# Optimization experiments

Measured on AMD Instinct MI355X. Metric: run time of the kernel, lower is better.

Reference implementation:

```python
import jax, jax.numpy as jnp
import numpy as np

B, N = 4, 1024                 # images, proposals per image
C_IN, POOL, HID = 256, 7, 1024
NUM_CLASSES = 21               # 20 fg + background (include_bg=False => +1)
FEAT_DIM = C_IN * POOL * POOL  # 12544
IMAGE_H = IMAGE_W = 800.0
STDS = np.array([0.1, 0.1, 0.2, 0.2], np.float32)
SCORE_THRESH = 0.1
NMS_THRESH = 0.5


def setup_inputs():
    key = jax.random.key(0)
    ks = jax.random.split(key, 11)
    props_feature = jax.random.normal(ks[0], (B * N, FEAT_DIM), jnp.float32)
    # well-formed xyxy proposals inside the image
    xy = jax.random.uniform(ks[1], (B, N, 2), minval=0.0, maxval=IMAGE_W - 64.0)
    wh = jax.random.uniform(ks[2], (B, N, 2), minval=8.0, maxval=256.0)
    proposals = jnp.concatenate([xy, jnp.minimum(xy + wh, IMAGE_W)], axis=-1)
    s = 0.02
    return {
        'props_feature': props_feature,
        'proposals': proposals,
        'fc6_w': jax.random.normal(ks[3], (FEAT_DIM, HID), jnp.float32) * s,
        'fc6_b': jnp.zeros((HID,), jnp.float32),
        'fc7_w': jax.random.normal(ks[4], (HID, HID), jnp.float32) * s,
        'fc7_b': jnp.zeros((HID,), jnp.float32),
        'cls_w': jax.random.normal(ks[5], (HID, NUM_CLASSES), jnp.float32) * s,
        'cls_b': jnp.zeros((NUM_CLASSES,), jnp.float32),
        'box_w': jax.random.normal(ks[6], (HID, NUM_CLASSES * 4), jnp.float32) * s,
        'box_b': jnp.zeros((NUM_CLASSES * 4,), jnp.float32),
    }


def _decode(deltas, props):
    # NormalizedProposalDecoder: deltas [...,4] (normalized), props xyxy [...,4]
    d = deltas * jnp.asarray(STDS)  # means are 0
    w = props[..., 2] - props[..., 0]
    h = props[..., 3] - props[..., 1]
    cx = props[..., 0] + 0.5 * w
    cy = props[..., 1] + 0.5 * h
    pcx = d[..., 0] * w + cx
    pcy = d[..., 1] * h + cy
    pw = jnp.exp(d[..., 2]) * w
    ph = jnp.exp(d[..., 3]) * h
    return jnp.stack([pcx - 0.5 * pw, pcy - 0.5 * ph,
                      pcx + 0.5 * pw, pcy + 0.5 * ph], axis=-1)


def _pairwise_iou(a, b):
    lt = jnp.maximum(a[:, None, :2], b[None, :, :2])
    rb = jnp.minimum(a[:, None, 2:], b[None, :, 2:])
    wh = jnp.maximum(rb - lt, 0.0)
    inter = wh[..., 0] * wh[..., 1]
    area_a = (a[:, 2] - a[:, 0]) * (a[:, 3] - a[:, 1])
    area_b = (b[:, 2] - b[:, 0]) * (b[:, 3] - b[:, 1])
    return inter / jnp.maximum(area_a[:, None] + area_b[None, :] - inter, 1e-9)


def _nms_keep(boxes, scores, labels, valid):
    # torchvision batched_nms: per-class via coordinate offset trick
    sc = jnp.where(valid, scores, -1.0)
    order = jnp.argsort(-sc)
    off = labels[order].astype(boxes.dtype)[:, None] * (IMAGE_W + 1.0)
    b = boxes[order] + off
    iou = _pairwise_iou(b, b)  # [N, N]
    idx = jnp.arange(N)

    def body(i, keep):
        sup = (iou[i] > NMS_THRESH) & keep[i] & (idx > i)
        return keep & ~sup

    keep_sorted = jax.lax.fori_loop(0, N, body, valid[order])
    return jnp.zeros(N, bool).at[order].set(keep_sorted)


def reference(props_feature, proposals, fc6_w, fc6_b, fc7_w, fc7_b,
              cls_w, cls_b, box_w, box_b):
    # TwoMLPHead
    x = jax.nn.relu(props_feature @ fc6_w + fc6_b)
    x = jax.nn.relu(x @ fc7_w + fc7_b)
    # FastRCNNPredictor
    scores = jax.nn.softmax(x @ cls_w + cls_b, axis=-1).reshape(B, N, NUM_CLASSES)
    deltas = (x @ box_w + box_b).reshape(B, N, NUM_CLASSES, 4)
    boxes = _decode(deltas, proposals[:, :, None, :])  # [B,N,C,4]
    # drop background column, keep per-box max-score class (scores == max mask)
    sc_fg = scores[..., 1:]
    bx_fg = boxes[:, :, 1:, :]
    best = jnp.argmax(sc_fg, axis=-1)                                  # [B,N]
    sc = jnp.take_along_axis(sc_fg, best[..., None], axis=-1)[..., 0]
    bx = jnp.take_along_axis(bx_fg, best[..., None, None], axis=-2)[..., 0, :]
    labels = best + 1
    # BBoxClipToImageSize
    hi = jnp.asarray([IMAGE_W, IMAGE_H, IMAGE_W, IMAGE_H], bx.dtype)
    bx = jnp.clip(bx, jnp.zeros(4, bx.dtype), hi)
    # BBoxSizeFilter(min=0) + score threshold
    valid = ((bx[..., 2] - bx[..., 0] > 0.0) & (bx[..., 3] - bx[..., 1] > 0.0)
             & (sc > SCORE_THRESH))
    keep = jax.vmap(_nms_keep)(bx, sc, labels, valid)                  # [B,N]
    res = jnp.concatenate([bx, (labels - 1).astype(bx.dtype)[..., None],
                           sc[..., None]], axis=-1)                    # [B,N,6]
    res = jnp.where(keep[..., None], res, 0.0)  # padded in place of ragged lists
    rpn_props = jnp.pad(proposals, ((0, 0), (0, 0), (0, 2)))
    rcnn_props = jnp.pad(bx, ((0, 0), (0, 0), (0, 2)))
    return res, keep, rpn_props, rcnn_props
```

## Files before the change

### kernel.cpp

```cpp
#include <hip/hip_runtime.h>
#include <hip/hip_bf16.h>

#define BATCH 4
#define NPROP 1024
#define HID 1024
#define NUM_CLASSES 21
#define FEAT_DIM 12544
#define NPB (BATCH * NPROP)
#define IMG 800.0f
#define SCORE_THRESH 0.1f
#define NMS_THRESH 0.5f
#define NCOL 112

typedef unsigned short u16;
typedef unsigned int u32;
typedef unsigned long long u64;
typedef short s16x8 __attribute__((ext_vector_type(8)));
typedef float f32x4 __attribute__((ext_vector_type(4)));

__device__ __forceinline__ void split2(float x0, float x1, u32& hp, u32& lp) {
    __hip_bfloat162 h2 = __float22bfloat162_rn(make_float2(x0, x1));
    u32 h = *(u32*)&h2;
    float f0 = __uint_as_float(h << 16);
    float f1 = __uint_as_float(h & 0xffff0000u);
    __hip_bfloat162 l2 = __float22bfloat162_rn(make_float2(x0 - f0, x1 - f1));
    hp = h;
    lp = *(u32*)&l2;
}

__device__ __forceinline__ size_t tile_off(int blk, int NTt, int t, int row, int g) {
    int r = row & 127;
    int c = r >> 4;
    int lanei = ((r & 15) << 2) | (g ^ ((r >> 1) & 3));
    return ((((size_t)blk * NTt + t) * 8 + c) << 9) + lanei * 8;
}

#define NB_WCAT 448
#define NB_T7C  256
#define NB_T6C  3136
#define NB_SPA  2048
#define NB_PREP (NB_WCAT + NB_T7C + NB_T6C + NB_SPA)

__device__ __forceinline__ void w_chunks(
    const float* __restrict__ W, u16* __restrict__ Th, u16* __restrict__ Tl,
    int NTt, int nb, int t, int tid, float (*lt)[129])
{
    const int n0 = nb * 128;
#pragma unroll
    for (int p = 0; p < 4; ++p) {
        int e = (p * 256 + tid) * 4;
        int k = e >> 7;
        int n = e & 127;
        float4 v = *(const float4*)(W + (size_t)(t * 32 + k) * 1024 + n0 + n);
        lt[k][n] = v.x; lt[k][n + 1] = v.y; lt[k][n + 2] = v.z; lt[k][n + 3] = v.w;
    }
    __syncthreads();
    const int lane = tid & 63, w = tid >> 6;
#pragma unroll
    for (int i = 0; i < 2; ++i) {
        const int c = w * 2 + i;
        const int rl = c * 16 + (lane >> 2);
        const int q = (lane & 3) ^ ((rl >> 1) & 3);
        u32 hp[4], lp[4];
#pragma unroll
        for (int e2 = 0; e2 < 4; ++e2)
            split2(lt[q * 8 + 2 * e2][rl], lt[q * 8 + 2 * e2 + 1][rl], hp[e2], lp[e2]);
        const size_t dsto = ((((size_t)nb * NTt + t) * 8 + c) << 9) + lane * 8;
        *(uint4*)&Th[dsto] = make_uint4(hp[0], hp[1], hp[2], hp[3]);
        *(uint4*)&Tl[dsto] = make_uint4(lp[0], lp[1], lp[2], lp[3]);
    }
    __syncthreads();
}

__global__ __launch_bounds__(256) void prep_kernel(
    const float* __restrict__ fc6_w, const float* __restrict__ fc7_w,
    const float* __restrict__ cls_w, const float* __restrict__ box_w,
    const float* __restrict__ A,
    u16* __restrict__ W6h, u16* __restrict__ W6l,
    u16* __restrict__ W7h, u16* __restrict__ W7l,
    float* __restrict__ Wcat, u16* __restrict__ A6h, u16* __restrict__ A6l)
{
    __shared__ float lt[32][129];
    const int b = blockIdx.x;
    const int tid = threadIdx.x;

    if (b < NB_WCAT) {
        int i = b * 256 + tid;
        if (i < HID * NCOL) {
            int k = i / NCOL, c = i % NCOL;
            float v = 0.0f;
            if (c < 21) v = cls_w[k * 21 + c];
            else if (c < 105) v = box_w[k * 84 + (c - 21)];
            Wcat[i] = v;
        }
    } else if (b < NB_WCAT + NB_T7C) {
        int idx = b - NB_WCAT;
        w_chunks(fc7_w, W7h, W7l, 32, idx / 32, idx % 32, tid, lt);
    } else if (b < NB_WCAT + NB_T7C + NB_T6C) {
        int idx = b - NB_WCAT - NB_T7C;
        w_chunks(fc6_w, W6h, W6l, 392, idx / 392, idx % 392, tid, lt);
    } else {
        const int sb = b - NB_WCAT - NB_T7C - NB_T6C;
        const int lane = tid & 63;
        const int w = tid >> 6;
        const int NCH = (NPB / 128) * (FEAT_DIM / 32) * 8;
        const int STRIDE = NB_SPA * 4;
        const int STRIDE4 = STRIDE * 4;

        auto srcaddr = [&](int ch) -> const float* {
            const int c = ch & 7;
            const int tmp = ch >> 3;
            const int t = tmp % (FEAT_DIM / 32);
            const int blk = tmp / (FEAT_DIM / 32);
            const int r = blk * 128 + c * 16 + (lane >> 2);
            const int col = t * 32 + (((lane & 3) ^ ((r >> 1) & 3)) << 3);
            return A + (size_t)r * FEAT_DIM + col;
        };
        auto proc = [&](int ch, const float4& xx, const float4& yy) {
            u32 hp0, hp1, hp2, hp3, lp0, lp1, lp2, lp3;
            split2(xx.x, xx.y, hp0, lp0);
            split2(xx.z, xx.w, hp1, lp1);
            split2(yy.x, yy.y, hp2, lp2);
            split2(yy.z, yy.w, hp3, lp3);
            const size_t dsto = ((size_t)ch << 9) + lane * 8;
            *(uint4*)&A6h[dsto] = make_uint4(hp0, hp1, hp2, hp3);
            *(uint4*)&A6l[dsto] = make_uint4(lp0, lp1, lp2, lp3);
        };

        int c0 = sb * 4 + w;
        int c1 = c0 + STRIDE;
        int c2 = c1 + STRIDE;
        int c3 = c2 + STRIDE;
        float4 x0{}, y0{}, x1{}, y1{}, x2{}, y2{}, x3{}, y3{};
        { const float* s = srcaddr(c0); x0 = *(const float4*)s; y0 = *(const float4*)(s + 4); }
        { const float* s = srcaddr(c1); x1 = *(const float4*)s; y1 = *(const float4*)(s + 4); }
        { const float* s = srcaddr(c2); x2 = *(const float4*)s; y2 = *(const float4*)(s + 4); }
        { const float* s = srcaddr(c3); x3 = *(const float4*)s; y3 = *(const float4*)(s + 4); }

        while (c0 < NCH || c1 < NCH || c2 < NCH || c3 < NCH) {
            if (c0 < NCH) {
                proc(c0, x0, y0);
                c0 += STRIDE4;
                if (c0 < NCH) { const float* s = srcaddr(c0); x0 = *(const float4*)s; y0 = *(const float4*)(s + 4); }
            }
            if (c1 < NCH) {
                proc(c1, x1, y1);
                c1 += STRIDE4;
                if (c1 < NCH) { const float* s = srcaddr(c1); x1 = *(const float4*)s; y1 = *(const float4*)(s + 4); }
            }
            if (c2 < NCH) {
                proc(c2, x2, y2);
                c2 += STRIDE4;
                if (c2 < NCH) { const float* s = srcaddr(c2); x2 = *(const float4*)s; y2 = *(const float4*)(s + 4); }
            }
            if (c3 < NCH) {
                proc(c3, x3, y3);
                c3 += STRIDE4;
                if (c3 < NCH) { const float* s = srcaddr(c3); x3 = *(const float4*)s; y3 = *(const float4*)(s + 4); }
            }
        }
    }
}

__global__ __launch_bounds__(256) void transpose_split(
    const float* __restrict__ W, u16* __restrict__ WhT, u16* __restrict__ WlT,
    int K, int N)
{
    __shared__ float tile[32][33];
    const int tid = threadIdx.x;
    const int n0 = blockIdx.x * 32;
    const int k0 = blockIdx.y * 32;
    {
        int i = tid >> 3, j4 = (tid & 7) * 4;
        float4 v = *(const float4*)(W + (size_t)(k0 + i) * N + n0 + j4);
        tile[i][j4] = v.x; tile[i][j4 + 1] = v.y; tile[i][j4 + 2] = v.z; tile[i][j4 + 3] = v.w;
    }
    __syncthreads();
    {
        int i = tid >> 3, j4 = (tid & 7) * 4;
        u32 hp0, lp0, hp1, lp1;
        split2(tile[j4 + 0][i], tile[j4 + 1][i], hp0, lp0);
        split2(tile[j4 + 2][i], tile[j4 + 3][i], hp1, lp1);
        size_t o = (size_t)(n0 + i) * K + k0 + j4;
        *(uint2*)&WhT[o] = make_uint2(hp0, hp1);
        *(uint2*)&WlT[o] = make_uint2(lp0, lp1);
    }
}

__global__ void build_wcat(const float* __restrict__ cls_w, const float* __restrict__ box_w,
                           float* __restrict__ Wcat)
{
    int i = blockIdx.x * 256 + threadIdx.x;
    if (i >= HID * NCOL) return;
    int k = i / NCOL, c = i % NCOL;
    float v = 0.0f;
    if (c < 21) v = cls_w[k * 21 + c];
    else if (c < 105) v = box_w[k * 84 + (c - 21)];
    Wcat[i] = v;
}

__global__ __launch_bounds__(256) void gemm_2ph_tiled(
    const u16* __restrict__ Ah, const u16* __restrict__ Al,
    const u16* __restrict__ Wh, const u16* __restrict__ Wl,
    const float* __restrict__ bias, float* __restrict__ Cout,
    int M, int Nn, int NTt, int tN, int mb0, int ymask, int bzshift)
{
    __shared__ u16 sm[2 * 16384];

    const int tid = threadIdx.x;
    const int lane = tid & 63;
    const int wv = tid >> 6;
    const int wr = wv >> 1, wc = wv & 1;

    const int flat = blockIdx.x + (blockIdx.y << 3) + blockIdx.z * 8 * gridDim.y;
    const int xcd = flat & 7;
    const int j = flat >> 3;
    const int bxi = j & 7;
    const int yy = (j >> 3) & ymask;
    const int bz = j >> bzshift;
    const int mb = mb0 + xcd * (ymask + 1) + yy;
    const int nb = bxi;
    const int bm = mb * 128, bn = nb * 128;
    const int t0 = bz * tN;

    const size_t abase = (size_t)mb * NTt * 4096;
    const size_t wbase = (size_t)nb * NTt * 4096;

    const int fr = lane & 15, fq = lane >> 4;
    int ia[4], ib[4];
#pragma unroll
    for (int m = 0; m < 4; ++m) {
        int ra = wr * 64 + m * 16 + fr;
        ia[m] = ra * 32 + ((fq ^ ((ra >> 1) & 3)) << 3);
        int rb = wc * 64 + m * 16 + fr;
        ib[m] = rb * 32 + ((fq ^ ((rb >> 1) & 3)) << 3);
    }

    f32x4 acc[4][4];
#pragma unroll
    for (int m = 0; m < 4; ++m)
#pragma unroll
        for (int n = 0; n < 4; ++n)
            acc[m][n] = (f32x4){0.f, 0.f, 0.f, 0.f};

    auto stage = [&](u16* dst, int t) {
#pragma unroll
        for (int i = 0; i < 2; ++i) {
            const int c = wv * 2 + i;
            const size_t so = (((size_t)t * 8 + c) << 9) + lane * 8;
            __builtin_amdgcn_global_load_lds(
                (const __attribute__((address_space(1))) u32*)(Ah + abase + so),
                (__attribute__((address_space(3))) u32*)(dst + c * 512), 16, 0, 0);
            __builtin_amdgcn_global_load_lds(
                (const __attribute__((address_space(1))) u32*)(Al + abase + so),
                (__attribute__((address_space(3))) u32*)(dst + 4096 + c * 512), 16, 0, 0);
            __builtin_amdgcn_global_load_lds(
                (const __attribute__((address_space(1))) u32*)(Wh + wbase + so),
                (__attribute__((address_space(3))) u32*)(dst + 8192 + c * 512), 16, 0, 0);
            __builtin_amdgcn_global_load_lds(
                (const __attribute__((address_space(1))) u32*)(Wl + wbase + so),
                (__attribute__((address_space(3))) u32*)(dst + 12288 + c * 512), 16, 0, 0);
        }
    };

    auto compute = [&](const u16* src) {
        s16x8 fah[4], fal[4], fbh[4], fbl[4];
#pragma unroll
        for (int m = 0; m < 4; ++m) {
            fah[m] = *(const s16x8*)&src[ia[m]];
            fal[m] = *(const s16x8*)&src[4096 + ia[m]];
            fbh[m] = *(const s16x8*)&src[8192 + ib[m]];
            fbl[m] = *(const s16x8*)&src[12288 + ib[m]];
        }
        __builtin_amdgcn_s_setprio(1);
#pragma unroll
        for (int m = 0; m < 4; ++m)
#pragma unroll
            for (int n = 0; n < 4; ++n) {
                acc[m][n] = __builtin_amdgcn_mfma_f32_16x16x32_bf16(fah[m], fbh[n], acc[m][n], 0, 0, 0);
                acc[m][n] = __builtin_amdgcn_mfma_f32_16x16x32_bf16(fah[m], fbl[n], acc[m][n], 0, 0, 0);
                acc[m][n] = __builtin_amdgcn_mfma_f32_16x16x32_bf16(fal[m], fbh[n], acc[m][n], 0, 0, 0);
            }
        __builtin_amdgcn_s_setprio(0);
    };

    u16* bufc = sm;
    u16* bufn = sm + 16384;

    stage(bufc, t0);
    for (int t = 0; t < tN; ++t) {
        if (t + 1 < tN) {
            stage(bufn, t0 + t + 1);
            asm volatile("s_waitcnt vmcnt(8)" ::: "memory");
        } else {
            asm volatile("s_waitcnt vmcnt(0)" ::: "memory");
        }
        asm volatile("s_barrier" ::: "memory");
        compute(bufc);
        asm volatile("s_barrier" ::: "memory");
        u16* tmp = bufc; bufc = bufn; bufn = tmp;
    }

    if (bias != nullptr) {
#pragma unroll
        for (int n = 0; n < 4; ++n) {
            int col = bn + wc * 64 + n * 16 + fr;
            float bb = bias[col];
#pragma unroll
            for (int m = 0; m < 4; ++m) {
                int row0 = bm + wr * 64 + m * 16 + fq * 4;
#pragma unroll
                for (int jj = 0; jj < 4; ++jj)
                    Cout[(size_t)(row0 + jj) * Nn + col] = fmaxf(acc[m][n][jj] + bb, 0.0f);
            }
        }
    } else {
        float* Cp = Cout + (size_t)bz * M * Nn;
#pragma unroll
        for (int n = 0; n < 4; ++n) {
            int col = bn + wc * 64 + n * 16 + fr;
#pragma unroll
            for (int m = 0; m < 4; ++m) {
                int row0 = bm + wr * 64 + m * 16 + fq * 4;
#pragma unroll
                for (int jj = 0; jj < 4; ++jj)
                    Cp[(size_t)(row0 + jj) * Nn + col] = acc[m][n][jj];
            }
        }
    }
}

__global__ __launch_bounds__(256) void gemm_2ph(
    const float* __restrict__ A, const u16* __restrict__ WhT, const u16* __restrict__ WlT,
    const float* __restrict__ bias, float* __restrict__ Cout,
    int M, int Nn, int K, int KC)
{
    __shared__ u16 sm[2 * 16384];

    const int tid = threadIdx.x;
    const int lane = tid & 63;
    const int wv = tid >> 6;
    const int wr = wv >> 1, wc = wv & 1;

    const int flat = blockIdx.x + (blockIdx.y << 3) + (blockIdx.z << 8);
    const int xcd = flat & 7;
    const int j = flat >> 3;
    const int bxi = j & 7;
    const int yy = (j >> 3) & 3;
    const int bz = j >> 5;
    const int bm = (xcd * 4 + yy) * 128;
    const int bn = bxi * 128;
    const int k0 = bz * KC;
    const int NT = KC / 32;

    const int ar = tid >> 1;
    const int ah = tid & 1;
    const float* aPtr = A + (size_t)(bm + ar) * K + ah * 16;
    const int asw = (ar >> 1) & 3;
    const int ac0 = ((2 * ah) ^ asw) << 3;
    const int ac1 = ((2 * ah + 1) ^ asw) << 3;

    int wrow[2], wlc[2];
#pragma unroll
    for (int i = 0; i < 2; ++i) {
        int c = wv * 2 + i;
        wrow[i] = c * 16 + (lane >> 2);
        wlc[i] = ((lane & 3) ^ ((wrow[i] >> 1) & 3)) * 8;
    }

    const int fr = lane & 15, fq = lane >> 4;
    int ia[4], ib[4];
#pragma unroll
    for (int m = 0; m < 4; ++m) {
        int ra = wr * 64 + m * 16 + fr;
        ia[m] = ra * 32 + ((fq ^ ((ra >> 1) & 3)) << 3);
        int rb = wc * 64 + m * 16 + fr;
        ib[m] = rb * 32 + ((fq ^ ((rb >> 1) & 3)) << 3);
    }

    f32x4 acc[4][4];
#pragma unroll
    for (int m = 0; m < 4; ++m)
#pragma unroll
        for (int n = 0; n < 4; ++n)
            acc[m][n] = (f32x4){0.f, 0.f, 0.f, 0.f};

    auto stage_w = [&](u16* dst, int kk) {
#pragma unroll
        for (int i = 0; i < 2; ++i) {
            const int c = wv * 2 + i;
            const u16* gh = WhT + (size_t)(bn + wrow[i]) * K + kk + wlc[i];
            const u16* gl = WlT + (size_t)(bn + wrow[i]) * K + kk + wlc[i];
            __builtin_amdgcn_global_load_lds(
                (const __attribute__((address_space(1))) u32*)gh,
                (__attribute__((address_space(3))) u32*)(dst + 8192 + c * 512), 16, 0, 0);
            __builtin_amdgcn_global_load_lds(
                (const __attribute__((address_space(1))) u32*)gl,
                (__attribute__((address_space(3))) u32*)(dst + 12288 + c * 512), 16, 0, 0);
        }
    };

    auto split_a = [&](u16* dst, float4 v0, float4 v1, float4 v2, float4 v3) {
        u32 hp[8], lp[8];
        split2(v0.x, v0.y, hp[0], lp[0]);
        split2(v0.z, v0.w, hp[1], lp[1]);
        split2(v1.x, v1.y, hp[2], lp[2]);
        split2(v1.z, v1.w, hp[3], lp[3]);
        split2(v2.x, v2.y, hp[4], lp[4]);
        split2(v2.z, v2.w, hp[5], lp[5]);
        split2(v3.x, v3.y, hp[6], lp[6]);
        split2(v3.z, v3.w, hp[7], lp[7]);
        *(uint4*)&dst[ar * 32 + ac0] = make_uint4(hp[0], hp[1], hp[2], hp[3]);
        *(uint4*)&dst[ar * 32 + ac1] = make_uint4(hp[4], hp[5], hp[6], hp[7]);
        *(uint4*)&dst[4096 + ar * 32 + ac0] = make_uint4(lp[0], lp[1], lp[2], lp[3]);
        *(uint4*)&dst[4096 + ar * 32 + ac1] = make_uint4(lp[4], lp[5], lp[6], lp[7]);
    };

    auto compute = [&](const u16* src) {
        s16x8 fah[4], fal[4], fbh[4], fbl[4];
#pragma unroll
        for (int m = 0; m < 4; ++m) {
            fah[m] = *(const s16x8*)&src[ia[m]];
            fal[m] = *(const s16x8*)&src[4096 + ia[m]];
            fbh[m] = *(const s16x8*)&src[8192 + ib[m]];
            fbl[m] = *(const s16x8*)&src[12288 + ib[m]];
        }
        __builtin_amdgcn_s_setprio(1);
#pragma unroll
        for (int m = 0; m < 4; ++m)
#pragma unroll
            for (int n = 0; n < 4; ++n) {
                acc[m][n] = __builtin_amdgcn_mfma_f32_16x16x32_bf16(fah[m], fbh[n], acc[m][n], 0, 0, 0);
                acc[m][n] = __builtin_amdgcn_mfma_f32_16x16x32_bf16(fah[m], fbl[n], acc[m][n], 0, 0, 0);
                acc[m][n] = __builtin_amdgcn_mfma_f32_16x16x32_bf16(fal[m], fbh[n], acc[m][n], 0, 0, 0);
            }
        __builtin_amdgcn_s_setprio(0);
    };

    u16* bufc = sm;
    u16* bufn = sm + 16384;

    stage_w(bufc, k0);
    {
        float4 a0 = *(const float4*)(aPtr + k0 + 0);
        float4 a1 = *(const float4*)(aPtr + k0 + 4);
        float4 a2 = *(const float4*)(aPtr + k0 + 8);
        float4 a3 = *(const float4*)(aPtr + k0 + 12);
        split_a(bufc, a0, a1, a2, a3);
    }
    asm volatile("s_waitcnt vmcnt(0) lgkmcnt(0)\n\ts_barrier" ::: "memory");

    for (int t = 0; t < NT; ++t) {
        float4 a0{}, a1{}, a2{}, a3{};
        const bool hn = (t + 1 < NT);
        if (hn) {
            const int kk = k0 + (t + 1) * 32;
            stage_w(bufn, kk);
            a0 = *(const float4*)(aPtr + kk + 0);
            a1 = *(const float4*)(aPtr + kk + 4);
            a2 = *(const float4*)(aPtr + kk + 8);
            a3 = *(const float4*)(aPtr + kk + 12);
        }
        compute(bufc);
        if (hn) split_a(bufn, a0, a1, a2, a3);
        asm volatile("s_waitcnt vmcnt(0) lgkmcnt(0)\n\ts_barrier" ::: "memory");
        u16* tmp = bufc; bufc = bufn; bufn = tmp;
    }

    if (bias != nullptr) {
#pragma unroll
        for (int n = 0; n < 4; ++n) {
            int col = bn + wc * 64 + n * 16 + fr;
            float bb = bias[col];
#pragma unroll
            for (int m = 0; m < 4; ++m) {
                int row0 = bm + wr * 64 + m * 16 + fq * 4;
#pragma unroll
                for (int jj = 0; jj < 4; ++jj)
                    Cout[(size_t)(row0 + jj) * Nn + col] = fmaxf(acc[m][n][jj] + bb, 0.0f);
            }
        }
    } else {
        float* Cp = Cout + (size_t)bz * M * Nn;
#pragma unroll
        for (int n = 0; n < 4; ++n) {
            int col = bn + wc * 64 + n * 16 + fr;
#pragma unroll
            for (int m = 0; m < 4; ++m) {
                int row0 = bm + wr * 64 + m * 16 + fq * 4;
#pragma unroll
                for (int jj = 0; jj < 4; ++jj)
                    Cp[(size_t)(row0 + jj) * Nn + col] = acc[m][n][jj];
            }
        }
    }
}

__global__ __launch_bounds__(256) void reduce_bias_relu(
    const float* __restrict__ Cpart, const float* __restrict__ bias,
    float* __restrict__ X, int MN, int Nn)
{
    const int total = MN / 4;
    for (int i4 = blockIdx.x * 256 + threadIdx.x; i4 < total; i4 += gridDim.x * 256) {
        const size_t o = (size_t)i4 * 4;
        float4 a = *(const float4*)(Cpart + o);
        float4 b = *(const float4*)(Cpart + (size_t)MN + o);
        float4 c = *(const float4*)(Cpart + 2 * (size_t)MN + o);
        float4 d = *(const float4*)(Cpart + 3 * (size_t)MN + o);
        float4 bb = *(const float4*)(bias + (o & (size_t)(Nn - 1)));
        float4 r;
        r.x = fmaxf(a.x + b.x + c.x + d.x + bb.x, 0.0f);
        r.y = fmaxf(a.y + b.y + c.y + d.y + bb.y, 0.0f);
        r.z = fmaxf(a.z + b.z + c.z + d.z + bb.z, 0.0f);
        r.w = fmaxf(a.w + b.w + c.w + d.w + bb.w, 0.0f);
        *(float4*)(X + o) = r;
    }
}

__global__ __launch_bounds__(256) void reduce_split_tiled(
    const float* __restrict__ Cpart, const float* __restrict__ bias,
    u16* __restrict__ Xh, u16* __restrict__ Xl, int MN, int Nn)
{
    const int total = MN / 8;
    for (int i = blockIdx.x * 256 + threadIdx.x; i < total; i += gridDim.x * 256) {
        const size_t o = (size_t)i * 8;
        float r8[8];
#pragma unroll
        for (int h = 0; h < 2; ++h) {
            float4 a = *(const float4*)(Cpart + o + h * 4);
            float4 b = *(const float4*)(Cpart + (size_t)MN + o + h * 4);
            float4 c = *(const float4*)(Cpart + 2 * (size_t)MN + o + h * 4);
            float4 d = *(const float4*)(Cpart + 3 * (size_t)MN + o + h * 4);
            float4 bb = *(const float4*)(bias + ((o + h * 4) & (size_t)(Nn - 1)));
            r8[h * 4 + 0] = fmaxf(a.x + b.x + c.x + d.x + bb.x, 0.0f);
            r8[h * 4 + 1] = fmaxf(a.y + b.y + c.y + d.y + bb.y, 0.0f);
            r8[h * 4 + 2] = fmaxf(a.z + b.z + c.z + d.z + bb.z, 0.0f);
            r8[h * 4 + 3] = fmaxf(a.w + b.w + c.w + d.w + bb.w, 0.0f);
        }
        u32 hp[4], lp[4];
#pragma unroll
        for (int t2 = 0; t2 < 4; ++t2)
            split2(r8[2 * t2], r8[2 * t2 + 1], hp[t2], lp[t2]);
        int row = (int)(o >> 10);
        int rem = (int)(o & 1023);
        int t = rem >> 5, g = (rem >> 3) & 3;
        size_t dsto = tile_off(row >> 7, 32, t, row, g);
        *(uint4*)&Xh[dsto] = make_uint4(hp[0], hp[1], hp[2], hp[3]);
        *(uint4*)&Xl[dsto] = make_uint4(lp[0], lp[1], lp[2], lp[3]);
    }
}

__global__ __launch_bounds__(256) void heads_postproc(
    const float* __restrict__ X2, const float* __restrict__ Wcat,
    const float* __restrict__ cls_b, const float* __restrict__ box_b,
    const float* __restrict__ proposals,
    float* __restrict__ bxo, float* __restrict__ sco,
    int* __restrict__ lbo, int* __restrict__ vdo)
{
    __shared__ float Xs[16][36];
    __shared__ float Ws[32 * NCOL];
    __shared__ float lgs[16][NCOL];
    const int tid = threadIdx.x;
    const int m0 = blockIdx.x * 16;
    const int tr = tid >> 4;
    const int tc = tid & 15;
    float acc[7] = {};
    for (int k0 = 0; k0 < HID; k0 += 32) {
        if (tid < 128) {
            int i = tid >> 3, j4 = (tid & 7) * 4;
            float4 v = *(const float4*)(X2 + (size_t)(m0 + i) * HID + k0 + j4);
            Xs[i][j4] = v.x; Xs[i][j4 + 1] = v.y; Xs[i][j4 + 2] = v.z; Xs[i][j4 + 3] = v.w;
        }
        const float4* src = (const float4*)(Wcat + (size_t)k0 * NCOL);
        float4* dst = (float4*)Ws;
        for (int i4 = tid; i4 < (32 * NCOL) / 4; i4 += 256) dst[i4] = src[i4];
        __syncthreads();
#pragma unroll 4
        for (int kk = 0; kk < 32; ++kk) {
            float a0 = Xs[tr][kk];
#pragma unroll
            for (int j = 0; j < 7; ++j)
                acc[j] = fmaf(a0, Ws[kk * NCOL + tc * 7 + j], acc[j]);
        }
        __syncthreads();
    }
#pragma unroll
    for (int j = 0; j < 7; ++j)
        lgs[tr][tc * 7 + j] = acc[j];
    __syncthreads();

    if (tid < 16) {
        const int p = m0 + tid;
        const float* lg = lgs[tid];
        float l[21];
        float m = -1e30f;
#pragma unroll
        for (int c = 0; c < 21; ++c) { l[c] = lg[c] + cls_b[c]; m = fmaxf(m, l[c]); }
        float e[21]; float s = 0.0f;
#pragma unroll
        for (int c = 0; c < 21; ++c) { e[c] = expf(l[c] - m); s += e[c]; }
        int best = 1;
#pragma unroll
        for (int c = 2; c < 21; ++c) if (e[c] > e[best]) best = c;
        const float score = e[best] / s;

        float d0 = (lg[21 + best * 4 + 0] + box_b[best * 4 + 0]) * 0.1f;
        float d1 = (lg[21 + best * 4 + 1] + box_b[best * 4 + 1]) * 0.1f;
        float d2 = (lg[21 + best * 4 + 2] + box_b[best * 4 + 2]) * 0.2f;
        float d3 = (lg[21 + best * 4 + 3] + box_b[best * 4 + 3]) * 0.2f;
        const float* pr = proposals + p * 4;
        float w_ = pr[2] - pr[0], h_ = pr[3] - pr[1];
        float cx = pr[0] + 0.5f * w_, cy = pr[1] + 0.5f * h_;
        float pcx = d0 * w_ + cx, pcy = d1 * h_ + cy;
        float pw = expf(d2) * w_, ph = expf(d3) * h_;
        float b0 = pcx - 0.5f * pw, b1 = pcy - 0.5f * ph;
        float b2 = pcx + 0.5f * pw, b3 = pcy + 0.5f * ph;
        b0 = fminf(fmaxf(b0, 0.0f), IMG);
        b1 = fminf(fmaxf(b1, 0.0f), IMG);
        b2 = fminf(fmaxf(b2, 0.0f), IMG);
        b3 = fminf(fmaxf(b3, 0.0f), IMG);
        int vd = (b2 - b0 > 0.0f) && (b3 - b1 > 0.0f) && (score > SCORE_THRESH);
        bxo[p * 4 + 0] = b0; bxo[p * 4 + 1] = b1;
        bxo[p * 4 + 2] = b2; bxo[p * 4 + 3] = b3;
        sco[p] = score;
        lbo[p] = best;
        vdo[p] = vd;
    }
}

__global__ __launch_bounds__(1024) void nms_finalize(
    const float* __restrict__ bx, const float* __restrict__ sc,
    const int* __restrict__ label, const int* __restrict__ valid,
    const float* __restrict__ proposals, float* __restrict__ out)
{
    const int img = blockIdx.x;
    const int base = img * NPROP;
    const int tid = threadIdx.x;
    const int lane = tid & 63;
    const int wv = tid >> 6;

    __shared__ u64 maskm[NPROP][16];
    __shared__ float4 sbx[NPROP];
    __shared__ float sarea[NPROP];
    __shared__ u64 kword[16];
    __shared__ int nv;

    u64* skey = &maskm[0][0];

    if (tid == 0) nv = 0;

    {
        float s = valid[base + tid] ? sc[base + tid] : -1.0f;
        unsigned u = __float_as_uint(s);
        u = (u & 0x80000000u) ? ~u : (u | 0x80000000u);
        u = ~u;
        skey[tid] = ((u64)u << 32) | (unsigned)tid;
    }
    for (int k = 2; k <= NPROP; k <<= 1) {
        for (int j = k >> 1; j > 0; j >>= 1) {
            __syncthreads();
            int ixj = tid ^ j;
            if (ixj > tid) {
                u64 a = skey[tid], b = skey[ixj];
                bool up = ((tid & k) == 0);
                if (up ? (a > b) : (a < b)) { skey[tid] = b; skey[ixj] = a; }
            }
        }
    }
    __syncthreads();

    const int myp = (int)(skey[tid] & 0xffffffffu);
    {
        float off = (float)label[base + myp] * (IMG + 1.0f);
        float x0 = bx[(base + myp) * 4 + 0] + off;
        float y0 = bx[(base + myp) * 4 + 1] + off;
        float x1 = bx[(base + myp) * 4 + 2] + off;
        float y1 = bx[(base + myp) * 4 + 3] + off;
        sbx[tid] = make_float4(x0, y0, x1, y1);
        sarea[tid] = (x1 - x0) * (y1 - y0);
        int v = valid[base + myp];
        u64 bb = __ballot(v != 0);
        if (lane == 0) kword[wv] = bb;
        if (v) atomicMax(&nv, tid + 1);
    }
    __syncthreads();
    const int nvalid = nv;

    for (int i = wv; i < nvalid; i += 16) {
        const float4 bi = sbx[i];
        const float ai = sarea[i];
#pragma unroll 4
        for (int w = 0; w < 16; ++w) {
            const int j = w * 64 + lane;
            bool sup = false;
            if (j > i && j < nvalid) {
                float4 bj = sbx[j];
                float lt0 = fmaxf(bi.x, bj.x);
                float lt1 = fmaxf(bi.y, bj.y);
                float rb0 = fminf(bi.z, bj.z);
                float rb1 = fminf(bi.w, bj.w);
                float w_ = fmaxf(rb0 - lt0, 0.0f);
                float h_ = fmaxf(rb1 - lt1, 0.0f);
                float inter = w_ * h_;
                float denom = fmaxf(ai + sarea[j] - inter, 1e-9f);
                sup = inter / denom > NMS_THRESH;
            }
            u64 bits = __ballot(sup);
            if (lane == 0) maskm[i][w] = bits;
        }
    }
    __syncthreads();

    if (tid < 64) {
        u64 kw = (tid < 16) ? kword[tid] : 0ull;
        u64 ra = 0, rb = 0, rc = 0, rd = 0;
        if (tid < 16) {
            if (0 < nvalid) ra = maskm[0][tid];
            if (1 < nvalid) rb = maskm[1][tid];
            if (2 < nvalid) rc = maskm[2][tid];
            if (3 < nvalid) rd = maskm[3][tid];
        }
        for (int i = 0; i < nvalid; i += 4) {
            {
                u64 srcw = __shfl(kw, i >> 6, 64);
                if ((srcw >> (i & 63)) & 1ull) { if (tid < 16) kw &= ~ra; }
                if (tid < 16 && i + 4 < nvalid) ra = maskm[i + 4][tid];
            }
            if (i + 1 < nvalid) {
                u64 srcw = __shfl(kw, (i + 1) >> 6, 64);
                if ((srcw >> ((i + 1) & 63)) & 1ull) { if (tid < 16) kw &= ~rb; }
                if (tid < 16 && i + 5 < nvalid) rb = maskm[i + 5][tid];
            }
            if (i + 2 < nvalid) {
                u64 srcw = __shfl(kw, (i + 2) >> 6, 64);
                if ((srcw >> ((i + 2) & 63)) & 1ull) { if (tid < 16) kw &= ~rc; }
                if (tid < 16 && i + 6 < nvalid) rc = maskm[i + 6][tid];
            }
            if (i + 3 < nvalid) {
                u64 srcw = __shfl(kw, (i + 3) >> 6, 64);
                if ((srcw >> ((i + 3) & 63)) & 1ull) { if (tid < 16) kw &= ~rd; }
                if (tid < 16 && i + 7 < nvalid) rd = maskm[i + 7][tid];
            }
        }
        if (tid < 16) kword[tid] = kw;
    }
    __syncthreads();

    {
        const int p = base + myp;
        const bool k = ((kword[tid >> 6] >> (tid & 63)) & 1ull) != 0;
        float* res   = out;
        float* keepo = out + NPB * 6;
        float* rpn   = keepo + NPB;
        float* rcnn  = rpn + NPB * 6;
        float b0 = bx[p * 4 + 0], b1 = bx[p * 4 + 1];
        float b2 = bx[p * 4 + 2], b3 = bx[p * 4 + 3];
        res[p * 6 + 0] = k ? b0 : 0.0f;
        res[p * 6 + 1] = k ? b1 : 0.0f;
        res[p * 6 + 2] = k ? b2 : 0.0f;
        res[p * 6 + 3] = k ? b3 : 0.0f;
        res[p * 6 + 4] = k ? (float)(label[p] - 1) : 0.0f;
        res[p * 6 + 5] = k ? sc[p] : 0.0f;
        keepo[p] = k ? 1.0f : 0.0f;
        rpn[p * 6 + 0] = proposals[p * 4 + 0];
        rpn[p * 6 + 1] = proposals[p * 4 + 1];
        rpn[p * 6 + 2] = proposals[p * 4 + 2];
        rpn[p * 6 + 3] = proposals[p * 4 + 3];
        rpn[p * 6 + 4] = 0.0f;
        rpn[p * 6 + 5] = 0.0f;
        rcnn[p * 6 + 0] = b0;
        rcnn[p * 6 + 1] = b1;
        rcnn[p * 6 + 2] = b2;
        rcnn[p * 6 + 3] = b3;
        rcnn[p * 6 + 4] = 0.0f;
        rcnn[p * 6 + 5] = 0.0f;
    }
}

extern "C" void kernel_launch(void* const* d_in, const int* in_sizes, int n_in,
                              void* d_out, int out_size, void* d_ws, size_t ws_size,
                              hipStream_t stream)
{
    const float* props_feature = (const float*)d_in[0];
    const float* proposals     = (const float*)d_in[1];
    const float* fc6_w         = (const float*)d_in[2];
    const float* fc6_b         = (const float*)d_in[3];
    const float* fc7_w         = (const float*)d_in[4];
    const float* fc7_b         = (const float*)d_in[5];
    const float* cls_w         = (const float*)d_in[6];
    const float* cls_b         = (const float*)d_in[7];
    const float* box_w         = (const float*)d_in[8];
    const float* box_b         = (const float*)d_in[9];
    float* out = (float*)d_out;

    char* ws = (char*)d_ws;
    float* X1     = (float*)(ws);
    float* X2     = (float*)(ws + 16777216);
    float* Wcat   = (float*)(ws + 33554432);
    float* bx     = (float*)(ws + 35848192);
    float* sc     = (float*)(ws + 35913728);
    int*   label  = (int*)  (ws + 35930112);
    int*   valid  = (int*)  (ws + 35946496);
    u16*   W6h    = (u16*)  (ws + 35979264);
    u16*   W6l    = (u16*)  (ws + 61669376);
    u16*   W7h    = (u16*)  (ws + 87359488);
    u16*   W7l    = (u16*)  (ws + 89456640);
    float* Cpart  = (float*)(ws + 91553792);
    u16*   A6h    = (u16*)  (ws + 158662656);
    u16*   A6l    = (u16*)  (ws + 261423104);
    u16*   X1h    = (u16*)  (ws + 364183552);
    u16*   X1l    = (u16*)  (ws + 372572160);
    const size_t NEED_SK   = 158662656ull;
    const size_t NEED_FULL = 380960768ull;

    if (ws_size >= NEED_FULL) {
        prep_kernel<<<NB_PREP, 256, 0, stream>>>(
            fc6_w, fc7_w, cls_w, box_w, props_feature,
            W6h, W6l, W7h, W7l, Wcat, A6h, A6l);
        gemm_2ph_tiled<<<dim3(8, 16, 4), 256, 0, stream>>>(
            A6h, A6l, W6h, W6l, nullptr, Cpart, NPB, HID, FEAT_DIM / 32, FEAT_DIM / 128,
            0, 1, 4);
        gemm_2ph_tiled<<<dim3(8, 16, 4), 256, 0, stream>>>(
            A6h, A6l, W6h, W6l, nullptr, Cpart, NPB, HID, FEAT_DIM / 32, FEAT_DIM / 128,
            16, 1, 4);
        reduce_split_tiled<<<1024, 256, 0, stream>>>(
            Cpart, fc6_b, X1h, X1l, NPB * HID, HID);
        gemm_2ph_tiled<<<dim3(8, 32, 1), 256, 0, stream>>>(
            X1h, X1l, W7h, W7l, fc7_b, X2, NPB, HID, HID / 32, HID / 32,
            0, 3, 5);
    } else if (ws_size >= NEED_SK) {
        build_wcat<<<(HID * NCOL + 255) / 256, 256, 0, stream>>>(cls_w, box_w, Wcat);
        transpose_split<<<dim3(HID / 32, FEAT_DIM / 32), 256, 0, stream>>>(
            fc6_w, W6h, W6l, FEAT_DIM, HID);
        transpose_split<<<dim3(HID / 32, HID / 32), 256, 0, stream>>>(
            fc7_w, W7h, W7l, HID, HID);
        gemm_2ph<<<dim3(8, 32, 4), 256, 0, stream>>>(
            props_feature, W6h, W6l, nullptr, Cpart, NPB, HID, FEAT_DIM, FEAT_DIM / 4);
        reduce_bias_relu<<<1024, 256, 0, stream>>>(Cpart, fc6_b, X1, NPB * HID, HID);
        gemm_2ph<<<dim3(8, 32, 1), 256, 0, stream>>>(
            X1, W7h, W7l, fc7_b, X2, NPB, HID, HID, HID);
    } else {
        build_wcat<<<(HID * NCOL + 255) / 256, 256, 0, stream>>>(cls_w, box_w, Wcat);
        transpose_split<<<dim3(HID / 32, FEAT_DIM / 32), 256, 0, stream>>>(
            fc6_w, W6h, W6l, FEAT_DIM, HID);
        transpose_split<<<dim3(HID / 32, HID / 32), 256, 0, stream>>>(
            fc7_w, W7h, W7l, HID, HID);
        gemm_2ph<<<dim3(8, 32, 1), 256, 0, stream>>>(
            props_feature, W6h, W6l, fc6_b, X1, NPB, HID, FEAT_DIM, FEAT_DIM);
        gemm_2ph<<<dim3(8, 32, 1), 256, 0, stream>>>(
            X1, W7h, W7l, fc7_b, X2, NPB, HID, HID, HID);
    }

    heads_postproc<<<NPB / 16, 256, 0, stream>>>(
        X2, Wcat, cls_b, box_b, proposals, bx, sc, label, valid);

    nms_finalize<<<BATCH, 1024, 0, stream>>>(bx, sc, label, valid, proposals, out);
}
```

Baseline: 655.4 us.

## Rebalance fc6 split-K to 2 and split-K fc7 with reduction fused into heads

The fc6 GEMM moves from two launches with 4-way split-K over 16 row tiles to a single launch with 2-way split-K over 32 row tiles, so the reduce kernel now sums only two partials. The fc7 GEMM also becomes 2-way split-K into the partial buffer. Its bias+ReLU reduction is folded into the heads kernel's activation load, which drops the X2 write and read. In exchange there are fewer K-slices per block for latency hiding, and the heads kernel reads two partial arrays instead of one.

```diff
diff --git a/kernel.cpp b/kernel.cpp
--- a/kernel.cpp
+++ b/kernel.cpp
@@ -517,7 +517,7 @@
     }
 }
 
-__global__ __launch_bounds__(256) void reduce_split_tiled(
+__global__ __launch_bounds__(256) void reduce2_split_tiled(
     const float* __restrict__ Cpart, const float* __restrict__ bias,
     u16* __restrict__ Xh, u16* __restrict__ Xl, int MN, int Nn)
 {
@@ -529,13 +529,11 @@
         for (int h = 0; h < 2; ++h) {
             float4 a = *(const float4*)(Cpart + o + h * 4);
             float4 b = *(const float4*)(Cpart + (size_t)MN + o + h * 4);
-            float4 c = *(const float4*)(Cpart + 2 * (size_t)MN + o + h * 4);
-            float4 d = *(const float4*)(Cpart + 3 * (size_t)MN + o + h * 4);
             float4 bb = *(const float4*)(bias + ((o + h * 4) & (size_t)(Nn - 1)));
-            r8[h * 4 + 0] = fmaxf(a.x + b.x + c.x + d.x + bb.x, 0.0f);
-            r8[h * 4 + 1] = fmaxf(a.y + b.y + c.y + d.y + bb.y, 0.0f);
-            r8[h * 4 + 2] = fmaxf(a.z + b.z + c.z + d.z + bb.z, 0.0f);
-            r8[h * 4 + 3] = fmaxf(a.w + b.w + c.w + d.w + bb.w, 0.0f);
+            r8[h * 4 + 0] = fmaxf(a.x + b.x + bb.x, 0.0f);
+            r8[h * 4 + 1] = fmaxf(a.y + b.y + bb.y, 0.0f);
+            r8[h * 4 + 2] = fmaxf(a.z + b.z + bb.z, 0.0f);
+            r8[h * 4 + 3] = fmaxf(a.w + b.w + bb.w, 0.0f);
         }
         u32 hp[4], lp[4];
 #pragma unroll
@@ -551,7 +549,9 @@
 }
 
 __global__ __launch_bounds__(256) void heads_postproc(
-    const float* __restrict__ X2, const float* __restrict__ Wcat,
+    const float* __restrict__ X2, const float* __restrict__ P,
+    const float* __restrict__ f7b, int fused,
+    const float* __restrict__ Wcat,
     const float* __restrict__ cls_b, const float* __restrict__ box_b,
     const float* __restrict__ proposals,
     float* __restrict__ bxo, float* __restrict__ sco,
@@ -564,11 +564,24 @@
     const int m0 = blockIdx.x * 16;
     const int tr = tid >> 4;
     const int tc = tid & 15;
+    const size_t MN = (size_t)NPB * HID;
     float acc[7] = {};
     for (int k0 = 0; k0 < HID; k0 += 32) {
         if (tid < 128) {
             int i = tid >> 3, j4 = (tid & 7) * 4;
-            float4 v = *(const float4*)(X2 + (size_t)(m0 + i) * HID + k0 + j4);
+            size_t off = (size_t)(m0 + i) * HID + k0 + j4;
+            float4 v;
+            if (fused) {
+                float4 a = *(const float4*)(P + off);
+                float4 b = *(const float4*)(P + MN + off);
+                float4 bb = *(const float4*)(f7b + k0 + j4);
+                v.x = fmaxf(a.x + b.x + bb.x, 0.0f);
+                v.y = fmaxf(a.y + b.y + bb.y, 0.0f);
+                v.z = fmaxf(a.z + b.z + bb.z, 0.0f);
+                v.w = fmaxf(a.w + b.w + bb.w, 0.0f);
+            } else {
+                v = *(const float4*)(X2 + off);
+            }
             Xs[i][j4] = v.x; Xs[i][j4 + 1] = v.y; Xs[i][j4 + 2] = v.z; Xs[i][j4 + 3] = v.w;
         }
         const float4* src = (const float4*)(Wcat + (size_t)k0 * NCOL);
@@ -817,17 +830,17 @@
         prep_kernel<<<NB_PREP, 256, 0, stream>>>(
             fc6_w, fc7_w, cls_w, box_w, props_feature,
             W6h, W6l, W7h, W7l, Wcat, A6h, A6l);
-        gemm_2ph_tiled<<<dim3(8, 16, 4), 256, 0, stream>>>(
-            A6h, A6l, W6h, W6l, nullptr, Cpart, NPB, HID, FEAT_DIM / 32, FEAT_DIM / 128,
-            0, 1, 4);
-        gemm_2ph_tiled<<<dim3(8, 16, 4), 256, 0, stream>>>(
-            A6h, A6l, W6h, W6l, nullptr, Cpart, NPB, HID, FEAT_DIM / 32, FEAT_DIM / 128,
-            16, 1, 4);
-        reduce_split_tiled<<<1024, 256, 0, stream>>>(
+        gemm_2ph_tiled<<<dim3(8, 32, 2), 256, 0, stream>>>(
+            A6h, A6l, W6h, W6l, nullptr, Cpart, NPB, HID, FEAT_DIM / 32, FEAT_DIM / 64,
+            0, 3, 5);
+        reduce2_split_tiled<<<1024, 256, 0, stream>>>(
             Cpart, fc6_b, X1h, X1l, NPB * HID, HID);
-        gemm_2ph_tiled<<<dim3(8, 32, 1), 256, 0, stream>>>(
-            X1h, X1l, W7h, W7l, fc7_b, X2, NPB, HID, HID / 32, HID / 32,
+        gemm_2ph_tiled<<<dim3(8, 32, 2), 256, 0, stream>>>(
+            X1h, X1l, W7h, W7l, nullptr, Cpart, NPB, HID, HID / 32, HID / 64,
             0, 3, 5);
+        heads_postproc<<<NPB / 16, 256, 0, stream>>>(
+            nullptr, Cpart, fc7_b, 1, Wcat, cls_b, box_b, proposals,
+            bx, sc, label, valid);
     } else if (ws_size >= NEED_SK) {
         build_wcat<<<(HID * NCOL + 255) / 256, 256, 0, stream>>>(cls_w, box_w, Wcat);
         transpose_split<<<dim3(HID / 32, FEAT_DIM / 32), 256, 0, stream>>>(
@@ -839,6 +852,9 @@
         reduce_bias_relu<<<1024, 256, 0, stream>>>(Cpart, fc6_b, X1, NPB * HID, HID);
         gemm_2ph<<<dim3(8, 32, 1), 256, 0, stream>>>(
             X1, W7h, W7l, fc7_b, X2, NPB, HID, HID, HID);
+        heads_postproc<<<NPB / 16, 256, 0, stream>>>(
+            X2, nullptr, nullptr, 0, Wcat, cls_b, box_b, proposals,
+            bx, sc, label, valid);
     } else {
         build_wcat<<<(HID * NCOL + 255) / 256, 256, 0, stream>>>(cls_w, box_w, Wcat);
         transpose_split<<<dim3(HID / 32, FEAT_DIM / 32), 256, 0, stream>>>(
@@ -849,10 +865,10 @@
             props_feature, W6h, W6l, fc6_b, X1, NPB, HID, FEAT_DIM, FEAT_DIM);
         gemm_2ph<<<dim3(8, 32, 1), 256, 0, stream>>>(
             X1, W7h, W7l, fc7_b, X2, NPB, HID, HID, HID);
-    }
-
-    heads_postproc<<<NPB / 16, 256, 0, stream>>>(
-        X2, Wcat, cls_b, box_b, proposals, bx, sc, label, valid);
+        heads_postproc<<<NPB / 16, 256, 0, stream>>>(
+            X2, nullptr, nullptr, 0, Wcat, cls_b, box_b, proposals,
+            bx, sc, label, valid);
+    }
 
     nms_finalize<<<BATCH, 1024, 0, stream>>>(bx, sc, label, valid, proposals, out);
 }
```

Result: faster. 641.4 us (-2.1%).
